# Kernel tuning notes

Hardware: AMD Instinct MI355X
Metric: run time of the kernel (lower is better)

The kernel has to match this reference:

```python
import jax, jax.numpy as jnp
import numpy as np


def setup_inputs() -> dict:
    key = jax.random.key(0)
    ks = jax.random.split(key, 6)
    B, HW, CIN, COUT, K = 256, 64, 3, 128, 32
    inputs = jax.random.normal(ks[0], (B, HW, HW, CIN), jnp.float32)
    conv_w = jax.random.normal(ks[1], (3, 3, CIN, COUT), jnp.float32) * 0.1
    conv_b = jnp.zeros((COUT,), jnp.float32)
    match_w = jax.random.normal(ks[2], (COUT,), jnp.float32) * 0.1
    match_b = jnp.zeros((1,), jnp.float32)
    pat_w = jax.random.normal(ks[3], (32 * 32 * K, 1), jnp.float32) * 0.01
    pat_b = jnp.zeros((1,), jnp.float32)
    base_w = jax.random.normal(ks[4], (32 * 32 * COUT, 3), jnp.float32) * 0.01
    base_b = jnp.zeros((3,), jnp.float32)
    pattern_set_index = jax.random.randint(ks[5], (K,), 0, COUT, jnp.int32)
    return {
        "inputs": inputs, "conv_w": conv_w, "conv_b": conv_b,
        "match_w": match_w, "match_b": match_b,
        "pat_w": pat_w, "pat_b": pat_b,
        "base_w": base_w, "base_b": base_b,
        "pattern_set_index": pattern_set_index,
    }


def reference(inputs, conv_w, conv_b, match_w, match_b,
              pat_w, pat_b, base_w, base_b, pattern_set_index):
    B = inputs.shape[0]
    # feat_extract: conv3x3 stride 2 + relu -> feats0 [B,32,32,128]; GAP -> feats1 [B,128]
    feats0 = jax.nn.relu(
        jax.lax.conv_general_dilated(
            inputs, conv_w, window_strides=(2, 2), padding='SAME',
            dimension_numbers=('NHWC', 'HWIO', 'NHWC')) + conv_b)
    feats1 = feats0.mean(axis=(1, 2))  # [B,128]
    # pat_matcher: boolean per-sample match mask
    matches = (feats1 @ match_w + match_b[0]) > 0.0  # [B] bool
    # pat_pred on channel-subset features (tf.gather axis=3)
    sel = jnp.take(feats0, pattern_set_index, axis=3)  # [B,32,32,32]
    p = jax.nn.sigmoid(sel.reshape(B, -1) @ pat_w + pat_b)[:, 0]  # [B]
    # BinaryToCategorical(pattern_class=0, num_classes=3): [p, (1-p)/2, (1-p)/2]
    o = (1.0 - p) * 0.5
    cat = jnp.stack([p, o, o], axis=-1)  # [B,3]
    # base_pred on full features (used for matched-low and non-matched samples)
    base = jax.nn.softmax(feats0.reshape(B, -1) @ base_w + base_b, axis=-1)  # [B,3]
    # route: matched AND pat score >= 0.5 -> categorized pat pred, else base pred
    use_pat = matches & (p >= 0.5)
    return jnp.where(use_pat[:, None], cat, base)
```

## Files before the change

### kernel.cpp

```cpp
#include <hip/hip_runtime.h>
#include <math.h>

#define TPB 1024

typedef float v2f __attribute__((ext_vector_type(2)));

__device__ float4 g_wq[131072];

__global__ __launch_bounds__(256)
void prep_weights(const float* __restrict__ base_w,
                  const float* __restrict__ pat_w,
                  const int*   __restrict__ psi)
{
    int idx = blockIdx.x * 256 + threadIdx.x;
    int hw = idx >> 7, c = idx & 127;
    const float* bp = base_w + (size_t)idx * 3;
    float b0 = bp[0], b1 = bp[1], b2 = bp[2];
    float pc = 0.f;
    const float* pr = pat_w + hw * 32;
    #pragma unroll
    for (int k = 0; k < 32; ++k)
        pc += (psi[k] == c) ? pr[k] : 0.f;
    g_wq[idx] = make_float4(b0, b1, b2, pc);
}

__global__ __launch_bounds__(TPB, 4)
void pattern_branch_kernel(const float* __restrict__ in,
                           const float* __restrict__ conv_w,
                           const float* __restrict__ conv_b,
                           const float* __restrict__ match_w,
                           const float* __restrict__ match_b,
                           const float* __restrict__ pat_b,
                           const float* __restrict__ base_b,
                           float* __restrict__ out)
{
    constexpr int ROWF4 = 50;
    __shared__ float4 xlds4[65 * ROWF4];
    __shared__ float  red[16][5];

    const int b   = blockIdx.x;
    const int tid = threadIdx.x;

    for (int s = tid; s < 65 * ROWF4; s += TPB) xlds4[s] = make_float4(0.f, 0.f, 0.f, 0.f);
    __syncthreads();
    const float4* inp4 = (const float4*)(in + (size_t)b * 12288);
    for (int s = tid; s < 64 * 48; s += TPB) {
        int r = s / 48;
        int q = s - r * 48;
        xlds4[r * ROWF4 + q] = inp4[s];
    }
    __syncthreads();

    const int lane31 = tid & 31;
    const int cg     = (tid >> 5) & 1;
    const int sg     = tid >> 6;
    const int c0     = lane31 + 32 * cg;
    v2f w2[27], bias2, mw2;
    bias2 = (v2f){ conv_b[c0],  conv_b[c0 + 64] };
    mw2   = (v2f){ match_w[c0], match_w[c0 + 64] };
    #pragma unroll
    for (int k = 0; k < 27; ++k)
        w2[k] = (v2f){ conv_w[k * 128 + c0], conv_w[k * 128 + c0 + 64] };

    v2f sm2  = (v2f){0.f, 0.f};
    v2f sb01 = (v2f){0.f, 0.f};
    v2f sb2p = (v2f){0.f, 0.f};

    for (int it = 0; it < 16; ++it) {
        int slot = it * 16 + sg;
        int oh = slot >> 3;
        int q  = slot & 7;
        v2f acc2[4];
        #pragma unroll
        for (int v = 0; v < 4; ++v) acc2[v] = bias2;

        #pragma unroll
        for (int kh = 0; kh < 3; ++kh) {
            float xr[28];
            const float4* rp = &xlds4[(2 * oh + kh) * ROWF4 + 6 * q];
            #pragma unroll
            for (int u = 0; u < 7; ++u) {
                float4 v4 = rp[u];
                xr[4*u] = v4.x; xr[4*u+1] = v4.y; xr[4*u+2] = v4.z; xr[4*u+3] = v4.w;
            }
            #pragma unroll
            for (int v = 0; v < 4; ++v)
                #pragma unroll
                for (int t9 = 0; t9 < 9; ++t9) {
                    float xv = xr[6 * v + t9];
                    int k = kh * 9 + t9;
                    acc2[v] = __builtin_elementwise_fma((v2f){xv, xv}, w2[k], acc2[v]);
                }
        }
        #pragma unroll
        for (int v = 0; v < 4; ++v) {
            int hw = oh * 32 + 4 * q + v;
            const float4* wqp = g_wq + hw * 128 + c0;
            v2f r2 = __builtin_elementwise_max(acc2[v], (v2f){0.f, 0.f});
            float4 wv0 = wqp[0];
            float4 wv1 = wqp[64];
            sm2  = __builtin_elementwise_fma(mw2, r2, sm2);
            sb01 = __builtin_elementwise_fma((v2f){r2.x, r2.x}, (v2f){wv0.x, wv0.y}, sb01);
            sb01 = __builtin_elementwise_fma((v2f){r2.y, r2.y}, (v2f){wv1.x, wv1.y}, sb01);
            sb2p = __builtin_elementwise_fma((v2f){r2.x, r2.x}, (v2f){wv0.z, wv0.w}, sb2p);
            sb2p = __builtin_elementwise_fma((v2f){r2.y, r2.y}, (v2f){wv1.z, wv1.w}, sb2p);
        }
    }

    float vals[5] = { sm2.x + sm2.y, sb01.x, sb01.y, sb2p.x, sb2p.y };
    #pragma unroll
    for (int off = 32; off > 0; off >>= 1)
        #pragma unroll
        for (int v = 0; v < 5; ++v)
            vals[v] += __shfl_down(vals[v], off, 64);
    int wv = tid >> 6, lane = tid & 63;
    if (lane == 0) {
        #pragma unroll
        for (int v = 0; v < 5; ++v) red[wv][v] = vals[v];
    }
    __syncthreads();
    if (tid == 0) {
        float t[5] = {0.f, 0.f, 0.f, 0.f, 0.f};
        for (int wj = 0; wj < 16; ++wj)
            #pragma unroll
            for (int v = 0; v < 5; ++v) t[v] += red[wj][v];
        float score = t[0] * (1.f / 1024.f) + match_b[0];
        float p = 1.f / (1.f + expf(-(t[4] + pat_b[0])));
        float l0 = t[1] + base_b[0], l1 = t[2] + base_b[1], l2 = t[3] + base_b[2];
        float m = fmaxf(l0, fmaxf(l1, l2));
        float e0 = expf(l0 - m), e1 = expf(l1 - m), e2 = expf(l2 - m);
        float inv = 1.f / (e0 + e1 + e2);
        bool use_pat = (score > 0.f) && (p >= 0.5f);
        float o0, o1, o2;
        if (use_pat) { o0 = p; o1 = 0.5f * (1.f - p); o2 = o1; }
        else         { o0 = e0 * inv; o1 = e1 * inv; o2 = e2 * inv; }
        out[b * 3 + 0] = o0;
        out[b * 3 + 1] = o1;
        out[b * 3 + 2] = o2;
    }
}

extern "C" void kernel_launch(void* const* d_in, const int* in_sizes, int n_in,
                              void* d_out, int out_size, void* d_ws, size_t ws_size,
                              hipStream_t stream) {
    const float* in      = (const float*)d_in[0];
    const float* conv_w  = (const float*)d_in[1];
    const float* conv_b  = (const float*)d_in[2];
    const float* match_w = (const float*)d_in[3];
    const float* match_b = (const float*)d_in[4];
    const float* pat_w   = (const float*)d_in[5];
    const float* pat_b   = (const float*)d_in[6];
    const float* base_w  = (const float*)d_in[7];
    const float* base_b  = (const float*)d_in[8];
    const int*   psi     = (const int*)d_in[9];
    float* out = (float*)d_out;

    (void)d_ws; (void)ws_size;

    prep_weights<<<512, 256, 0, stream>>>(base_w, pat_w, psi);

    int B = in_sizes[0] / (64 * 64 * 3);
    pattern_branch_kernel<<<B, TPB, 0, stream>>>(
        in, conv_w, conv_b, match_w, match_b, pat_b, base_b, out);
}
```

Before: 123.0 us.

## Map threads to output pixels and loop over channel pairs with transposed weights

Each thread now owns one output pixel, keeping its 3x3x3 input patch in registers, and loops over 64 channel pairs. Conv weights, bias and match weights are packed per channel pair into a global table, and the base/pattern weights are transposed to channel-major order so each pair's loads are coalesced across threads. This removes the repeated LDS row reads per slot. In exchange, every thread reads the same uniform weight values from global memory on each iteration, and the 27 FMAs per pair are split across two accumulators.

Result: no change. 123.7 us (+0.6%).

```diff
diff --git a/kernel.cpp b/kernel.cpp
--- a/kernel.cpp
+++ b/kernel.cpp
@@ -1,110 +1,101 @@
 #include <hip/hip_runtime.h>
 #include <math.h>
 
-#define TPB 1024
-
 typedef float v2f __attribute__((ext_vector_type(2)));
 
-__device__ float4 g_wq[131072];
+__device__ float4 g_wqt[131072];
+__device__ v2f g_cwt[64 * 29];
 
 __global__ __launch_bounds__(256)
 void prep_weights(const float* __restrict__ base_w,
                   const float* __restrict__ pat_w,
-                  const int*   __restrict__ psi)
+                  const int*   __restrict__ psi,
+                  const float* __restrict__ conv_w,
+                  const float* __restrict__ conv_b,
+                  const float* __restrict__ match_w)
 {
     int idx = blockIdx.x * 256 + threadIdx.x;
-    int hw = idx >> 7, c = idx & 127;
-    const float* bp = base_w + (size_t)idx * 3;
-    float b0 = bp[0], b1 = bp[1], b2 = bp[2];
+    int c = idx >> 10, hw = idx & 1023;
+    const float* bp = base_w + ((size_t)hw * 128 + c) * 3;
     float pc = 0.f;
     const float* pr = pat_w + hw * 32;
     #pragma unroll
     for (int k = 0; k < 32; ++k)
         pc += (psi[k] == c) ? pr[k] : 0.f;
-    g_wq[idx] = make_float4(b0, b1, b2, pc);
+    g_wqt[idx] = make_float4(bp[0], bp[1], bp[2], pc);
+
+    if (idx < 64 * 29) {
+        int p = idx / 29, r = idx - p * 29;
+        v2f v;
+        if (r < 27)       v = (v2f){ conv_w[r * 128 + 2 * p], conv_w[r * 128 + 2 * p + 1] };
+        else if (r == 27) v = (v2f){ conv_b[2 * p], conv_b[2 * p + 1] };
+        else              v = (v2f){ match_w[2 * p], match_w[2 * p + 1] };
+        g_cwt[idx] = v;
+    }
 }
 
-__global__ __launch_bounds__(TPB, 4)
+__global__ __launch_bounds__(1024, 4)
 void pattern_branch_kernel(const float* __restrict__ in,
-                           const float* __restrict__ conv_w,
-                           const float* __restrict__ conv_b,
-                           const float* __restrict__ match_w,
                            const float* __restrict__ match_b,
                            const float* __restrict__ pat_b,
                            const float* __restrict__ base_b,
                            float* __restrict__ out)
 {
-    constexpr int ROWF4 = 50;
-    __shared__ float4 xlds4[65 * ROWF4];
-    __shared__ float  red[16][5];
+    __shared__ float xf[65 * 200];
+    __shared__ float red[16][5];
 
     const int b   = blockIdx.x;
     const int tid = threadIdx.x;
 
-    for (int s = tid; s < 65 * ROWF4; s += TPB) xlds4[s] = make_float4(0.f, 0.f, 0.f, 0.f);
+    float4* x4 = (float4*)xf;
+    for (int s = tid; s < 65 * 50; s += 1024) x4[s] = make_float4(0.f, 0.f, 0.f, 0.f);
     __syncthreads();
     const float4* inp4 = (const float4*)(in + (size_t)b * 12288);
-    for (int s = tid; s < 64 * 48; s += TPB) {
+    for (int s = tid; s < 64 * 48; s += 1024) {
         int r = s / 48;
         int q = s - r * 48;
-        xlds4[r * ROWF4 + q] = inp4[s];
+        x4[r * 50 + q] = inp4[s];
     }
     __syncthreads();
 
-    const int lane31 = tid & 31;
-    const int cg     = (tid >> 5) & 1;
-    const int sg     = tid >> 6;
-    const int c0     = lane31 + 32 * cg;
-    v2f w2[27], bias2, mw2;
-    bias2 = (v2f){ conv_b[c0],  conv_b[c0 + 64] };
-    mw2   = (v2f){ match_w[c0], match_w[c0 + 64] };
+    const int oh = tid >> 5;
+    const int ow = tid & 31;
+    v2f xs[15];
     #pragma unroll
-    for (int k = 0; k < 27; ++k)
-        w2[k] = (v2f){ conv_w[k * 128 + c0], conv_w[k * 128 + c0 + 64] };
+    for (int kh = 0; kh < 3; ++kh) {
+        int rowoff = (2 * oh + kh) * 200 + 6 * ow;
+        #pragma unroll
+        for (int u = 0; u < 5; ++u)
+            xs[kh * 5 + u] = *(const v2f*)&xf[rowoff + 2 * u];
+    }
 
     v2f sm2  = (v2f){0.f, 0.f};
     v2f sb01 = (v2f){0.f, 0.f};
     v2f sb2p = (v2f){0.f, 0.f};
 
-    for (int it = 0; it < 16; ++it) {
-        int slot = it * 16 + sg;
-        int oh = slot >> 3;
-        int q  = slot & 7;
-        v2f acc2[4];
+    for (int p = 0; p < 64; ++p) {
+        const v2f* wp = g_cwt + p * 29;
+        v2f accA = wp[27];
+        v2f accB = (v2f){0.f, 0.f};
         #pragma unroll
-        for (int v = 0; v < 4; ++v) acc2[v] = bias2;
+        for (int kh = 0; kh < 3; ++kh)
+            #pragma unroll
+            for (int t9 = 0; t9 < 9; ++t9) {
+                float xv = xs[kh * 5 + (t9 >> 1)][t9 & 1];
+                v2f wv = wp[kh * 9 + t9];
+                if (t9 & 1) accB = __builtin_elementwise_fma((v2f){xv, xv}, wv, accB);
+                else        accA = __builtin_elementwise_fma((v2f){xv, xv}, wv, accA);
+            }
+        v2f f2 = __builtin_elementwise_max(accA + accB, (v2f){0.f, 0.f});
 
-        #pragma unroll
-        for (int kh = 0; kh < 3; ++kh) {
-            float xr[28];
-            const float4* rp = &xlds4[(2 * oh + kh) * ROWF4 + 6 * q];
-            #pragma unroll
-            for (int u = 0; u < 7; ++u) {
-                float4 v4 = rp[u];
-                xr[4*u] = v4.x; xr[4*u+1] = v4.y; xr[4*u+2] = v4.z; xr[4*u+3] = v4.w;
-            }
-            #pragma unroll
-            for (int v = 0; v < 4; ++v)
-                #pragma unroll
-                for (int t9 = 0; t9 < 9; ++t9) {
-                    float xv = xr[6 * v + t9];
-                    int k = kh * 9 + t9;
-                    acc2[v] = __builtin_elementwise_fma((v2f){xv, xv}, w2[k], acc2[v]);
-                }
-        }
-        #pragma unroll
-        for (int v = 0; v < 4; ++v) {
-            int hw = oh * 32 + 4 * q + v;
-            const float4* wqp = g_wq + hw * 128 + c0;
-            v2f r2 = __builtin_elementwise_max(acc2[v], (v2f){0.f, 0.f});
-            float4 wv0 = wqp[0];
-            float4 wv1 = wqp[64];
-            sm2  = __builtin_elementwise_fma(mw2, r2, sm2);
-            sb01 = __builtin_elementwise_fma((v2f){r2.x, r2.x}, (v2f){wv0.x, wv0.y}, sb01);
-            sb01 = __builtin_elementwise_fma((v2f){r2.y, r2.y}, (v2f){wv1.x, wv1.y}, sb01);
-            sb2p = __builtin_elementwise_fma((v2f){r2.x, r2.x}, (v2f){wv0.z, wv0.w}, sb2p);
-            sb2p = __builtin_elementwise_fma((v2f){r2.y, r2.y}, (v2f){wv1.z, wv1.w}, sb2p);
-        }
+        float4 wv0 = g_wqt[(2 * p) * 1024 + tid];
+        float4 wv1 = g_wqt[(2 * p + 1) * 1024 + tid];
+        v2f mw2 = wp[28];
+        sm2  = __builtin_elementwise_fma(mw2, f2, sm2);
+        sb01 = __builtin_elementwise_fma((v2f){f2.x, f2.x}, (v2f){wv0.x, wv0.y}, sb01);
+        sb01 = __builtin_elementwise_fma((v2f){f2.y, f2.y}, (v2f){wv1.x, wv1.y}, sb01);
+        sb2p = __builtin_elementwise_fma((v2f){f2.x, f2.x}, (v2f){wv0.z, wv0.w}, sb2p);
+        sb2p = __builtin_elementwise_fma((v2f){f2.y, f2.y}, (v2f){wv1.z, wv1.w}, sb2p);
     }
 
     float vals[5] = { sm2.x + sm2.y, sb01.x, sb01.y, sb2p.x, sb2p.y };
@@ -157,9 +148,9 @@
 
     (void)d_ws; (void)ws_size;
 
-    prep_weights<<<512, 256, 0, stream>>>(base_w, pat_w, psi);
+    prep_weights<<<512, 256, 0, stream>>>(base_w, pat_w, psi, conv_w, conv_b, match_w);
 
     int B = in_sizes[0] / (64 * 64 * 3);
-    pattern_branch_kernel<<<B, TPB, 0, stream>>>(
-        in, conv_w, conv_b, match_w, match_b, pat_b, base_b, out);
+    pattern_branch_kernel<<<B, 1024, 0, stream>>>(
+        in, match_b, pat_b, base_b, out);
 }
```
